# Kernel tuning notes

Measured on AMD Instinct MI355X. Metric: run time of the kernel, lower is better.

Reference implementation:

```python
import jax, jax.numpy as jnp
import numpy as np

B, IN_SEQ, TGT_SEQ = 128, 50, 25
IN_SIZE, OUT_SIZE, RNN = 128, 128, 2048


def setup_inputs() -> dict:
    key = jax.random.key(0)
    ks = jax.random.split(key, 10)
    s_in = 1.0 / np.sqrt(IN_SIZE)
    s_out = 1.0 / np.sqrt(OUT_SIZE)
    s_rnn = 1.0 / np.sqrt(RNN)
    return {
        "encoder_inputs": jax.random.normal(ks[0], (B, IN_SEQ, IN_SIZE), jnp.float32),
        "decoder_inputs": jax.random.normal(ks[1], (B, TGT_SEQ, IN_SIZE), jnp.float32),
        "fc1_w": jax.random.uniform(ks[2], (OUT_SIZE, IN_SIZE), jnp.float32, -s_in, s_in),
        "fc1_b": jax.random.uniform(ks[3], (OUT_SIZE,), jnp.float32, -s_in, s_in),
        "w_ih": jax.random.uniform(ks[4], (3 * RNN, OUT_SIZE), jnp.float32, -s_rnn, s_rnn),
        "w_hh": jax.random.uniform(ks[5], (3 * RNN, RNN), jnp.float32, -s_rnn, s_rnn),
        "b_ih": jax.random.uniform(ks[6], (3 * RNN,), jnp.float32, -s_rnn, s_rnn),
        "b_hh": jax.random.uniform(ks[7], (3 * RNN,), jnp.float32, -s_rnn, s_rnn),
        "fc2_w": jax.random.uniform(ks[8], (OUT_SIZE, RNN), jnp.float32, -s_rnn, s_rnn),
        "fc2_b": jax.random.uniform(ks[9], (OUT_SIZE,), jnp.float32, -s_rnn, s_rnn),
    }


def _gru_cell(x, h, w_ih, w_hh, b_ih, b_hh):
    # PyTorch GRUCell: gates ordered (r, z, n)
    gi = x @ w_ih.T + b_ih            # [B, 3R]
    gh = h @ w_hh.T + b_hh            # [B, 3R]
    i_r, i_z, i_n = jnp.split(gi, 3, axis=-1)
    h_r, h_z, h_n = jnp.split(gh, 3, axis=-1)
    r = jax.nn.sigmoid(i_r + h_r)
    z = jax.nn.sigmoid(i_z + h_z)
    n = jnp.tanh(i_n + r * h_n)
    return (1.0 - z) * n + z * h


def reference(encoder_inputs, decoder_inputs, fc1_w, fc1_b, w_ih, w_hh, b_ih, b_hh, fc2_w, fc2_b):
    # Eval mode: F.dropout(training=False) is identity.
    enc = encoder_inputs @ fc1_w.T + fc1_b              # [B, S_in, OUT]
    enc_t = jnp.transpose(enc, (1, 0, 2))               # time-major [S_in, B, OUT]
    h0 = jnp.zeros((encoder_inputs.shape[0], RNN), enc.dtype)

    def enc_step(state, x):
        return _gru_cell(x, state, w_ih, w_hh, b_ih, b_hh), None

    state, _ = jax.lax.scan(enc_step, h0, enc_t[:-1])   # input_seq - 1 steps

    def dec_step(carry, _):
        state, inp = carry
        inp = jax.lax.stop_gradient(inp)                # inp.detach()
        state = _gru_cell(inp, state, w_ih, w_hh, b_ih, b_hh)
        out = inp + state @ fc2_w.T + fc2_b             # residual decoder
        return (state, out), out

    _, outs = jax.lax.scan(dec_step, (state, enc_t[-1]), None, length=TGT_SEQ)
    return jnp.transpose(outs, (1, 0, 2))               # [B, TGT_SEQ, OUT]
```

## Files before the change

### kernel.cpp

```cpp
#include <hip/hip_runtime.h>
#include <limits.h>

constexpr int kB   = 128;
constexpr int kSin = 50;
constexpr int kT   = 25;
constexpr int kD   = 128;
constexpr int kR   = 2048;
constexpr int kNB  = 256;
constexpr int kNT  = 512;

typedef __bf16 bf16x8 __attribute__((ext_vector_type(8)));
typedef float  f32x4  __attribute__((ext_vector_type(4)));
typedef unsigned short u16;
typedef unsigned long long u64;

__device__ __forceinline__ float bf2f(u16 u){ union{unsigned i; float f;}x; x.i=((unsigned)u)<<16; return x.f; }
__device__ __forceinline__ u16 f2bf(float f){ union{float f; unsigned i;}x; x.f=f; return (u16)((x.i + 0x7FFFu + ((x.i>>16)&1u))>>16); }
__device__ __forceinline__ float sigm(float x){ return 1.f/(1.f+__expf(-x)); }

__device__ __forceinline__ void stg32(unsigned* p, unsigned v){
    __hip_atomic_store(p, v, __ATOMIC_RELAXED, __HIP_MEMORY_SCOPE_AGENT);
}
__device__ __forceinline__ void stg64(u64* p, u64 v){
    __hip_atomic_store(p, v, __ATOMIC_RELAXED, __HIP_MEMORY_SCOPE_AGENT);
}
__device__ __forceinline__ unsigned ald32(const void* p){
    return __hip_atomic_load((const unsigned*)p, __ATOMIC_RELAXED, __HIP_MEMORY_SCOPE_AGENT);
}
__device__ __forceinline__ u64 ald64(const void* p){
    return __hip_atomic_load((const u64*)p, __ATOMIC_RELAXED, __HIP_MEMORY_SCOPE_AGENT);
}
__device__ __forceinline__ bf16x8 ald128bf(const u16* p){
    union{ u64 q[2]; bf16x8 v; } t;
    t.q[0] = ald64(p);
    t.q[1] = ald64(p + 4);
    return t.v;
}
__device__ __forceinline__ float aldf(const float* p){
    union{ unsigned u; float f; } t; t.u = ald32(p); return t.f;
}

__device__ __forceinline__ bf16x8 pack8(float4 a, float4 b){
    union{ bf16x8 v; u16 u[8]; } t;
    t.u[0]=f2bf(a.x); t.u[1]=f2bf(a.y); t.u[2]=f2bf(a.z); t.u[3]=f2bf(a.w);
    t.u[4]=f2bf(b.x); t.u[5]=f2bf(b.y); t.u[6]=f2bf(b.z); t.u[7]=f2bf(b.w);
    return t.v;
}

__device__ __forceinline__ int pollflag(int* flags, int idx, int iter){
    if ((iter & 31) == 31) return atomicMax(&flags[idx*16], INT_MIN);
    return (int)ald32(&flags[idx*16]);
}
__device__ __forceinline__ void wait16(int* flags, int k, int base){
    const int lane = threadIdx.x & 63;
    for (int iter = 0;; ++iter){
        bool ok = true;
        if (lane < 16) ok = (pollflag(flags, base + lane, iter) >= k);
        if (__ballot(ok) == ~0ull) return;
        __builtin_amdgcn_s_sleep(1);
    }
}
__device__ __forceinline__ void wait128(int* flags, int k, int base){
    const int lane = threadIdx.x & 63;
    for (int iter = 0;; ++iter){
        bool ok = true;
#pragma unroll
        for (int j = 0; j < 2; ++j)
            ok &= (pollflag(flags, base + lane*2 + j, iter) >= k);
        if (__ballot(ok) == ~0ull) return;
        __builtin_amdgcn_s_sleep(1);
    }
}
__device__ __forceinline__ void arrive(int* flags, int k){
    __syncthreads();
    if (threadIdx.x == 0) atomicMax(&flags[blockIdx.x*16], k);
}

__device__ __forceinline__ void gbar(int* flags, int k, int base, int perlane)
{
    __syncthreads();
    const int tid = threadIdx.x;
    if (tid == 0) atomicMax(&flags[blockIdx.x*16], k);
    if (tid < 64) {
        int iter = 0;
        for (;;) {
            bool ok = true;
            for (int j = 0; j < perlane; ++j) {
                const int idx = base + tid*perlane + j;
                int v;
                if ((iter & 31) == 31) v = atomicMax(&flags[idx*16], INT_MIN);
                else                   v = (int)ald32(&flags[idx*16]);
                ok &= (v >= k);
            }
            if (__ballot(ok) == ~0ull) break;
            ++iter;
            __builtin_amdgcn_s_sleep(1);
        }
    }
    __syncthreads();
}

__device__ __forceinline__ void cvt_f32_bf16(const float* __restrict__ s, u16* __restrict__ d,
                                             int n4, int gtid, int gstride)
{
    for (int i = gtid; i < n4; i += gstride) {
        float4 v = ((const float4*)s)[i];
        u64 pk = (u64)f2bf(v.x) | ((u64)f2bf(v.y)<<16) | ((u64)f2bf(v.z)<<32) | ((u64)f2bf(v.w)<<48);
        stg64((u64*)d + i, pk);
    }
}

template<int NT, int NACC>
__device__ __forceinline__ void small_gemm(
    const u16* __restrict__ Am, int alda,
    const u16* __restrict__ Bp, int bldb,
    f32x4 (&acc)[NACC], u16* pool)
{
    const int tid=threadIdx.x, lane=tid&63, wv=tid>>6, g=wv>>2, mt=wv&3, ar=lane&15, aq=lane>>4;
    u16* sA = pool;
    u16* sB = pool + 8704;
    { int q=tid,     r=q>>4, c=q&15; *(uint4*)&sA[r*136+c*8] = *(const uint4*)(Am + r*alda + c*8); }
    { int q=tid+512, r=q>>4, c=q&15; *(uint4*)&sA[r*136+c*8] = *(const uint4*)(Am + r*alda + c*8); }
    for (int q=tid; q<NT*256; q+=kNT){
        int r=q>>4, c=q&15;
        *(uint4*)&sB[r*136+c*8] = *(const uint4*)(Bp + (size_t)r*bldb + c*8);
    }
    __syncthreads();
#pragma unroll
    for (int jt=0; jt<NT; ++jt){
        if ((jt&1) != g) continue;
#pragma unroll
        for (int kk=0; kk<4; ++kk){
            bf16x8 a = *(const bf16x8*)&sA[(mt*16+ar)*136 + kk*32 + aq*8];
            bf16x8 b = *(const bf16x8*)&sB[(jt*16+ar)*136 + kk*32 + aq*8];
            acc[jt>>1] = __builtin_amdgcn_mfma_f32_16x16x32_bf16(a,b,acc[jt>>1],0,0,0);
        }
    }
    __syncthreads();
}

__device__ __forceinline__ void gru_phase_flag(
    const u16* __restrict__ hcur, u16* __restrict__ hnxt,
    const u16* __restrict__ xb,
    const bf16x8 (&wB)[3][8], const bf16x8 (&wI)[3],
    const float4 b4, float (&hprev)[4],
    int wgc, int mrow0, u16* smem, u16* sH,
    int* flags, int hk, int xk, int fbase)
{
    const int tid=threadIdx.x, lane=tid&63, w=tid>>6, ar=lane&15, aq=lane>>4;
    const f32x4 zz = {0.f,0.f,0.f,0.f};
    f32x4 acc[3][4] = {{zz,zz,zz,zz},{zz,zz,zz,zz},{zz,zz,zz,zz}};
    f32x4 xn[4] = {zz,zz,zz,zz};

    if (hk) wait16(flags, hk, fbase + 16*w);

#pragma unroll
    for (int mt=0; mt<4; ++mt){
        const int row = mrow0 + mt*16 + ar;
        bf16x8 af[8];
#pragma unroll
        for (int c=0; c<8; ++c){
            const int s = 16*w + 2*c + (aq>>1);
            af[c] = ald128bf(hcur + (((s*128 + row)<<4) + (aq&1)*8));
        }
#pragma unroll
        for (int c=0; c<8; ++c){
            acc[0][mt] = __builtin_amdgcn_mfma_f32_16x16x32_bf16(af[c], wB[0][c], acc[0][mt],0,0,0);
            acc[1][mt] = __builtin_amdgcn_mfma_f32_16x16x32_bf16(af[c], wB[1][c], acc[1][mt],0,0,0);
            acc[2][mt] = __builtin_amdgcn_mfma_f32_16x16x32_bf16(af[c], wB[2][c], acc[2][mt],0,0,0);
        }
    }
    if (w < 4){
        if (xk) wait128(flags, xk, fbase);
#pragma unroll
        for (int mt=0; mt<4; ++mt){
            bf16x8 ax = ald128bf(xb + (mrow0+mt*16+ar)*kD + 32*w + aq*8);
            acc[0][mt] = __builtin_amdgcn_mfma_f32_16x16x32_bf16(ax, wI[0], acc[0][mt],0,0,0);
            acc[1][mt] = __builtin_amdgcn_mfma_f32_16x16x32_bf16(ax, wI[1], acc[1][mt],0,0,0);
            xn[mt]     = __builtin_amdgcn_mfma_f32_16x16x32_bf16(ax, wI[2], xn[mt],0,0,0);
        }
    }
    float* red = (float*)smem;
#define RCELL(wp,g4,mt) (red + (((((wp)*4+(g4))*4+(mt))*64 + lane)<<2))
    if (w >= 4){
#pragma unroll
        for (int g=0; g<3; ++g)
#pragma unroll
            for (int mt=0; mt<4; ++mt)
                *(f32x4*)RCELL(w-4, g, mt) = acc[g][mt];
    }
    __syncthreads();
    if (w < 4){
#pragma unroll
        for (int g=0; g<3; ++g)
#pragma unroll
            for (int mt=0; mt<4; ++mt)
                acc[g][mt] += *(f32x4*)RCELL(w, g, mt);
#pragma unroll
        for (int g=0; g<3; ++g)
#pragma unroll
            for (int mt=0; mt<4; ++mt)
                *(f32x4*)RCELL(w, g, mt) = acc[g][mt];
#pragma unroll
        for (int mt=0; mt<4; ++mt)
            *(f32x4*)RCELL(w, 3, mt) = xn[mt];
    }
    __syncthreads();
    if (tid < 256){
        const int mt = tid>>6, ls = tid&63, aqs = ls>>4, ars = ls&15;
        f32x4 R=zz, Z=zz, NH=zz, NX=zz;
#pragma unroll
        for (int wp=0; wp<4; ++wp){
            R  += *(f32x4*)(red + ((((wp*4+0)*4+mt)*64 + ls)<<2));
            Z  += *(f32x4*)(red + ((((wp*4+1)*4+mt)*64 + ls)<<2));
            NH += *(f32x4*)(red + ((((wp*4+2)*4+mt)*64 + ls)<<2));
            NX += *(f32x4*)(red + ((((wp*4+3)*4+mt)*64 + ls)<<2));
        }
#pragma unroll
        for (int rr=0; rr<4; ++rr){
            const int m = mrow0 + mt*16 + aqs*4 + rr;
            float r_ = sigm(R[rr] + b4.x);
            float z_ = sigm(Z[rr] + b4.y);
            float n_ = tanhf(NX[rr] + b4.z + r_*(NH[rr] + b4.w));
            float hn = (1.f-z_)*n_ + z_*hprev[rr];
            hprev[rr] = hn;
            u16 hb = f2bf(hn);
            sH[(mt*16 + aqs*4 + rr)*16 + ars] = hb;
            unsigned other = (unsigned)__shfl_xor((int)(unsigned)hb, 1);
            if (!(ars&1))
                stg32((unsigned*)(hnxt + ((wgc*128+m)<<4) + ars), (unsigned)hb | (other<<16));
        }
    }
#undef RCELL
    __syncthreads();
}

__device__ __forceinline__ void fc2_partial(
    const u16* __restrict__ sH, const bf16x8 (&wF2)[4],
    int wgc, int mh, float* __restrict__ part)
{
    const int tid=threadIdx.x, lane=tid&63, w=tid>>6, ar=lane&15, aq=lane>>4;
    const int mt = w&3, nh = w>>2;
    bf16x8 a;
    if (aq < 2) a = *(const bf16x8*)&sH[(mt*16+ar)*16 + aq*8];
    else {
#pragma unroll
        for (int i=0;i<8;++i) a[i] = (__bf16)0.f;
    }
    const f32x4 zz = {0.f,0.f,0.f,0.f};
    f32x4 acc[4] = {zz,zz,zz,zz};
#pragma unroll
    for (int j=0;j<4;++j)
        acc[j] = __builtin_amdgcn_mfma_f32_16x16x32_bf16(a, wF2[j], acc[j],0,0,0);
#pragma unroll
    for (int j=0;j<4;++j){
        const int col = (nh*4+j)*16 + ar;
#pragma unroll
        for (int rr=0;rr<4;++rr){
            const int row = mt*16 + aq*4 + rr;
            stg32((unsigned*)(part + ((((size_t)mh*64+row)*128 + wgc)*128 + col)),
                  __float_as_uint(acc[j][rr]));
        }
    }
}

__global__ __launch_bounds__(kNT, 2) void seq2seq_kernel(
    const void* __restrict__ enc_in_raw, const void* __restrict__ fc1_w_raw,
    const void* __restrict__ fc1_b_raw,  const void* __restrict__ w_ih_raw,
    const void* __restrict__ w_hh_raw,   const void* __restrict__ b_ih_raw,
    const void* __restrict__ b_hh_raw,   const void* __restrict__ fc2_w_raw,
    const void* __restrict__ fc2_b_raw,
    void* __restrict__ out_raw,
    u16* __restrict__ enc_act,
    u16* __restrict__ h_b16,
    u16* __restrict__ inp_b16,
    float* __restrict__ inp_f32,
    float* __restrict__ encF,
    float* __restrict__ bias,
    float* __restrict__ part,
    int* flags,
    u16* __restrict__ cv_encx, u16* __restrict__ cv_fc2, u16* __restrict__ cv_fc1)
{
    __shared__ __align__(16) u16 smem[33792];
    __shared__ int sflag;
    u16* sH = smem + 32768;
    const int wg = blockIdx.x, tid = threadIdx.x;
    const int wgc = wg & 127, mrow0 = (wg >> 7) * 64;
    const int lane = tid & 63, wv = tid >> 6, ar = lane & 15, aq = lane >> 4;
    const int gtid = wg * kNT + tid, gstride = kNB * kNT;
    const int dom = (wg >> 7) * 128;

    {
        const u16* p = (const u16*)enc_in_raw;
        int found = 0;
        for (int i = tid; i < 16384; i += kNT) found |= ((p[i] & 0x7F80) == 0x7F80) ? 1 : 0;
        if (tid == 0) sflag = 0;
        __syncthreads();
        if (found) sflag = 1;
        __syncthreads();
    }
    const bool F32 = (sflag != 0);

    bf16x8 wB[3][8];
    bf16x8 wI[3];
    {
        const int w4 = wv & 3;
        if (F32){
            const float* Wh = (const float*)w_hh_raw;
            const float* Wi = (const float*)w_ih_raw;
#pragma unroll
            for (int g=0; g<3; ++g)
#pragma unroll
                for (int c=0; c<8; ++c){
                    size_t o = (size_t)(g*kR + wgc*16 + ar)*kR + 256*wv + 32*c + aq*8;
                    wB[g][c] = pack8(*(const float4*)(Wh+o), *(const float4*)(Wh+o+4));
                }
#pragma unroll
            for (int g=0; g<3; ++g){
                size_t o = (size_t)(g*kR + wgc*16 + ar)*kD + 32*w4 + aq*8;
                wI[g] = pack8(*(const float4*)(Wi+o), *(const float4*)(Wi+o+4));
            }
        } else {
            const u16* Wh = (const u16*)w_hh_raw;
            const u16* Wi = (const u16*)w_ih_raw;
#pragma unroll
            for (int g=0; g<3; ++g)
#pragma unroll
                for (int c=0; c<8; ++c)
                    wB[g][c] = *(const bf16x8*)(Wh + (size_t)(g*kR + wgc*16 + ar)*kR + 256*wv + 32*c + aq*8);
#pragma unroll
            for (int g=0; g<3; ++g)
                wI[g] = *(const bf16x8*)(Wi + (size_t)(g*kR + wgc*16 + ar)*kD + 32*w4 + aq*8);
        }
    }

    if (F32) {
        cvt_f32_bf16((const float*)fc2_w_raw, cv_fc2,  (kD*kR)/4,       gtid, gstride);
        cvt_f32_bf16((const float*)fc1_w_raw, cv_fc1,  (kD*kD)/4,       gtid, gstride);
        cvt_f32_bf16((const float*)enc_in_raw,cv_encx, (kB*kSin*kD)/4,  gtid, gstride);
        for (int i = gtid; i < 3*kR; i += gstride) {
            stg32((unsigned*)&bias[i],        __float_as_uint(((const float*)b_ih_raw)[i]));
            stg32((unsigned*)&bias[3*kR + i], __float_as_uint(((const float*)b_hh_raw)[i]));
        }
        for (int i = gtid; i < kD; i += gstride) {
            stg32((unsigned*)&bias[6*kR + i],      __float_as_uint(((const float*)fc1_b_raw)[i]));
            stg32((unsigned*)&bias[6*kR + kD + i], __float_as_uint(((const float*)fc2_b_raw)[i]));
        }
    } else {
        for (int i = gtid; i < 3*kR; i += gstride) {
            stg32((unsigned*)&bias[i],        __float_as_uint(bf2f(((const u16*)b_ih_raw)[i])));
            stg32((unsigned*)&bias[3*kR + i], __float_as_uint(bf2f(((const u16*)b_hh_raw)[i])));
        }
        for (int i = gtid; i < kD; i += gstride) {
            stg32((unsigned*)&bias[6*kR + i],      __float_as_uint(bf2f(((const u16*)fc1_b_raw)[i])));
            stg32((unsigned*)&bias[6*kR + kD + i], __float_as_uint(bf2f(((const u16*)fc2_b_raw)[i])));
        }
    }
    for (int i = gtid; i < (kB*kR)/2; i += gstride) stg32((unsigned*)h_b16 + i, 0u);
    gbar(flags, 1, 0, 4);

    const u16* ENCX = F32 ? cv_encx : (const u16*)enc_in_raw;
    const u16* WF2  = F32 ? cv_fc2  : (const u16*)fc2_w_raw;
    const u16* WF1  = F32 ? cv_fc1  : (const u16*)fc1_w_raw;

    float4 b4;
    {
        const int hc = wgc*16 + ar;
        b4.x = aldf(&bias[hc])      + aldf(&bias[3*kR+hc]);
        b4.y = aldf(&bias[kR+hc])   + aldf(&bias[4*kR+hc]);
        b4.z = aldf(&bias[2*kR+hc]);
        b4.w = aldf(&bias[5*kR+hc]);
    }
    bf16x8 wF2[4];
    {
        const int nh = wv>>2;
#pragma unroll
        for (int j=0;j<4;++j){
            if (aq < 2)
                wF2[j] = ald128bf(WF2 + (size_t)((nh*4+j)*16+ar)*kR + wgc*16 + aq*8);
            else {
#pragma unroll
                for (int i=0;i<8;++i) wF2[j][i] = (__bf16)0.f;
            }
        }
    }
    const float fc2b = aldf(&bias[6*kR + kD + (wg&1)*64 + (tid&63)]);
    float hprev[4] = {0.f, 0.f, 0.f, 0.f};

    if (wgc < kSin) {
        const int g = wv>>2, mt = wv&3;
        const f32x4 zz = {0.f,0.f,0.f,0.f};
        f32x4 ae[4] = {zz,zz,zz,zz};
        small_gemm<8,4>(ENCX + ((size_t)mrow0*kSin + wgc)*kD, kSin*kD, WF1, kD, ae, smem);
#pragma unroll
        for (int jt=0; jt<8; ++jt){
            if ((jt&1) != g) continue;
            int col = jt*16 + ar;
            float fb = aldf(&bias[6*kR + col]);
#pragma unroll
            for (int rr=0; rr<4; ++rr){
                int m = mrow0 + mt*16 + aq*4 + rr;
                float v = ae[jt>>1][rr] + fb;
                u16 hb = f2bf(v);
                unsigned other = (unsigned)__shfl_xor((int)(unsigned)hb, 1);
                if (!(ar&1))
                    stg32((unsigned*)(enc_act + ((size_t)wgc*kB + m)*kD + col),
                          (unsigned)hb | (other<<16));
                if (wgc == kSin-1)
                    stg32((unsigned*)(encF + (size_t)m*kD + col), __float_as_uint(v));
            }
        }
    }
    gbar(flags, 2, dom, 2);

    int par = 0;
    for (int t = 0; t < kSin-1; ++t) {
        gru_phase_flag(h_b16 + (size_t)par*kB*kR, h_b16 + (size_t)(1-par)*kB*kR,
                       enc_act + (size_t)t*kB*kD, wB, wI, b4, hprev, wgc, mrow0, smem, sH,
                       flags, (t==0 ? 0 : t+2), 0, dom);
        arrive(flags, t+3);
        par ^= 1;
    }

    const u16*   ib  = enc_act + (size_t)(kSin-1)*kB*kD;
    const float* ifp = encF;
    const int mh = wg >> 7;
    for (int d = 0; d < kT; ++d) {
        gru_phase_flag(h_b16 + (size_t)par*kB*kR, h_b16 + (size_t)(1-par)*kB*kR,
                       ib, wB, wI, b4, hprev, wgc, mrow0, smem, sH,
                       flags, (d==0 ? 51 : 50+2*d), (d==0 ? 0 : 51+2*d), dom);
        fc2_partial(sH, wF2, wgc, mh, part);
        arrive(flags, 52+2*d);
        par ^= 1;

        u16*   nib = inp_b16 + (size_t)(d&1)*kB*kD;
        float* nif = inp_f32 + (size_t)(d&1)*kB*kD;
        wait128(flags, 52+2*d, dom);
        {
            const int row = wg >> 1, ch = wg & 1;
            const int mh2 = row >> 6, rl = row & 63;
            const float* pr = part + (size_t)((mh2*64 + rl)*128)*128;
            const int cl = tid & 63, sg = tid >> 6;
            float s = 0.f;
#pragma unroll
            for (int j=0;j<16;++j) s += aldf(&pr[(size_t)(sg*16+j)*128 + ch*64 + cl]);
            float* red2 = (float*)smem;
            red2[sg*64 + cl] = s;
            __syncthreads();
            if (tid < 64){
                float t2 = 0.f;
#pragma unroll
                for (int g2=0; g2<8; ++g2) t2 += red2[g2*64 + tid];
                const int colg = ch*64 + tid;
                const float o = t2 + fc2b + aldf(&ifp[(size_t)row*kD + colg]);
                const size_t ob = ((size_t)row*kT + d)*kD + colg;
                if (F32) ((float*)out_raw)[ob] = o;
                else     ((u16*)out_raw)[ob]   = f2bf(o);
                stg32((unsigned*)(nif + (size_t)row*kD + colg), __float_as_uint(o));
                u16 hb = f2bf(o);
                unsigned other = (unsigned)__shfl_xor((int)(unsigned)hb, 1);
                if (!(tid&1))
                    stg32((unsigned*)(nib + (size_t)row*kD + colg), (unsigned)hb | (other<<16));
            }
        }
        arrive(flags, 53+2*d);
        ib = nib; ifp = nif;
    }
}

extern "C" void kernel_launch(void* const* d_in, const int* in_sizes, int n_in,
                              void* d_out, int out_size, void* d_ws, size_t ws_size,
                              hipStream_t stream)
{
    size_t off = 0;
    char* ws = (char*)d_ws;
    auto alloc = [&](size_t bytes) -> char* {
        char* p = ws + off;
        off = (off + bytes + 255) & ~(size_t)255;
        return p;
    };
    u16*   enc_act = (u16*)alloc((size_t)kSin*kB*kD*2);
    u16*   h_b16   = (u16*)alloc((size_t)2*kB*kR*2);
    u16*   inp_b16 = (u16*)alloc((size_t)2*kB*kD*2);
    float* inp_f32 = (float*)alloc((size_t)2*kB*kD*4);
    float* encF    = (float*)alloc((size_t)kB*kD*4);
    float* bias    = (float*)alloc((size_t)(6*kR + 2*kD)*4);
    float* part    = (float*)alloc((size_t)2*64*128*128*4);
    int*   flags   = (int*)alloc((size_t)kNB*16*4);
    u16*   cv_encx = (u16*)alloc((size_t)kB*kSin*kD*2);
    u16*   cv_fc2  = (u16*)alloc((size_t)kD*kR*2);
    u16*   cv_fc1  = (u16*)alloc((size_t)kD*kD*2);
    (void)ws_size; (void)in_sizes; (void)n_in; (void)out_size;

    seq2seq_kernel<<<dim3(kNB), dim3(kNT), 0, stream>>>(
        d_in[0], d_in[2], d_in[3], d_in[4], d_in[5], d_in[6], d_in[7], d_in[8], d_in[9],
        d_out,
        enc_act, h_b16, inp_b16, inp_f32, encF, bias, part, flags,
        cv_encx, cv_fc2, cv_fc1);
}
```

Baseline: 1.537 ms.

## Use 8-slot hidden-state ring with plain loads and periodic acquire fences

Switches the hidden-state and decoder-input double buffers to an 8-deep ring. This lets the per-step hidden and input reads use ordinary cached vector loads instead of relaxed agent-scope atomic loads, with an acquire fence only when the ring wraps. The aim is to cut the latency of the atomic 128-bit loads on the critical recurrent path. The risk is correctness: this relies on stale cache lines never being hit for fresh slots. Only the ring zero slot is initialized, and the flag waits themselves may not order the plain loads.

```diff
diff --git a/kernel.cpp b/kernel.cpp
--- a/kernel.cpp
+++ b/kernel.cpp
@@ -8,6 +8,7 @@
 constexpr int kR   = 2048;
 constexpr int kNB  = 256;
 constexpr int kNT  = 512;
+constexpr int kRing = 8;
 
 typedef __bf16 bf16x8 __attribute__((ext_vector_type(8)));
 typedef float  f32x4  __attribute__((ext_vector_type(4)));
@@ -145,13 +146,15 @@
     const bf16x8 (&wB)[3][8], const bf16x8 (&wI)[3],
     const float4 b4, float (&hprev)[4],
     int wgc, int mrow0, u16* smem, u16* sH,
-    int* flags, int hk, int xk, int fbase)
+    int* flags, int hk, int xk, int fbase, bool dofence)
 {
     const int tid=threadIdx.x, lane=tid&63, w=tid>>6, ar=lane&15, aq=lane>>4;
     const f32x4 zz = {0.f,0.f,0.f,0.f};
     f32x4 acc[3][4] = {{zz,zz,zz,zz},{zz,zz,zz,zz},{zz,zz,zz,zz}};
     f32x4 xn[4] = {zz,zz,zz,zz};
 
+    if (dofence) __builtin_amdgcn_fence(__ATOMIC_ACQUIRE, "agent");
+
     if (hk) wait16(flags, hk, fbase + 16*w);
 
 #pragma unroll
@@ -161,7 +164,7 @@
 #pragma unroll
         for (int c=0; c<8; ++c){
             const int s = 16*w + 2*c + (aq>>1);
-            af[c] = ald128bf(hcur + (((s*128 + row)<<4) + (aq&1)*8));
+            af[c] = *(const bf16x8*)(hcur + (((s*128 + row)<<4) + (aq&1)*8));
         }
 #pragma unroll
         for (int c=0; c<8; ++c){
@@ -174,7 +177,7 @@
         if (xk) wait128(flags, xk, fbase);
 #pragma unroll
         for (int mt=0; mt<4; ++mt){
-            bf16x8 ax = ald128bf(xb + (mrow0+mt*16+ar)*kD + 32*w + aq*8);
+            bf16x8 ax = *(const bf16x8*)(xb + (mrow0+mt*16+ar)*kD + 32*w + aq*8);
             acc[0][mt] = __builtin_amdgcn_mfma_f32_16x16x32_bf16(ax, wI[0], acc[0][mt],0,0,0);
             acc[1][mt] = __builtin_amdgcn_mfma_f32_16x16x32_bf16(ax, wI[1], acc[1][mt],0,0,0);
             xn[mt]     = __builtin_amdgcn_mfma_f32_16x16x32_bf16(ax, wI[2], xn[mt],0,0,0);
@@ -289,6 +292,7 @@
     const int lane = tid & 63, wv = tid >> 6, ar = lane & 15, aq = lane >> 4;
     const int gtid = wg * kNT + tid, gstride = kNB * kNT;
     const int dom = (wg >> 7) * 128;
+    const size_t HS = (size_t)kB*kR;
 
     {
         const u16* p = (const u16*)enc_in_raw;
@@ -356,7 +360,7 @@
             stg32((unsigned*)&bias[6*kR + kD + i], __float_as_uint(bf2f(((const u16*)fc2_b_raw)[i])));
         }
     }
-    for (int i = gtid; i < (kB*kR)/2; i += gstride) stg32((unsigned*)h_b16 + i, 0u);
+    for (int i = gtid; i < (int)((kB*kR)/2); i += gstride) stg32((unsigned*)h_b16 + i, 0u);
     gbar(flags, 1, 0, 4);
 
     const u16* ENCX = F32 ? cv_encx : (const u16*)enc_in_raw;
@@ -413,28 +417,28 @@
     }
     gbar(flags, 2, dom, 2);
 
-    int par = 0;
     for (int t = 0; t < kSin-1; ++t) {
-        gru_phase_flag(h_b16 + (size_t)par*kB*kR, h_b16 + (size_t)(1-par)*kB*kR,
+        gru_phase_flag(h_b16 + (size_t)(t & 7)*HS, h_b16 + (size_t)((t+1) & 7)*HS,
                        enc_act + (size_t)t*kB*kD, wB, wI, b4, hprev, wgc, mrow0, smem, sH,
-                       flags, (t==0 ? 0 : t+2), 0, dom);
+                       flags, (t==0 ? 0 : t+2), 0, dom,
+                       (t > 0) && ((t & 7) == 0));
         arrive(flags, t+3);
-        par ^= 1;
     }
 
     const u16*   ib  = enc_act + (size_t)(kSin-1)*kB*kD;
     const float* ifp = encF;
     const int mh = wg >> 7;
     for (int d = 0; d < kT; ++d) {
-        gru_phase_flag(h_b16 + (size_t)par*kB*kR, h_b16 + (size_t)(1-par)*kB*kR,
+        const int g = 49 + d;
+        gru_phase_flag(h_b16 + (size_t)(g & 7)*HS, h_b16 + (size_t)((g+1) & 7)*HS,
                        ib, wB, wI, b4, hprev, wgc, mrow0, smem, sH,
-                       flags, (d==0 ? 51 : 50+2*d), (d==0 ? 0 : 51+2*d), dom);
+                       flags, (d==0 ? 51 : 50+2*d), (d==0 ? 0 : 51+2*d), dom,
+                       (g & 7) == 0);
         fc2_partial(sH, wF2, wgc, mh, part);
         arrive(flags, 52+2*d);
-        par ^= 1;
-
-        u16*   nib = inp_b16 + (size_t)(d&1)*kB*kD;
-        float* nif = inp_f32 + (size_t)(d&1)*kB*kD;
+
+        u16*   nib = inp_b16 + (size_t)(d & 7)*kB*kD;
+        float* nif = inp_f32 + (size_t)(d & 7)*kB*kD;
         wait128(flags, 52+2*d, dom);
         {
             const int row = wg >> 1, ch = wg & 1;
@@ -452,7 +456,7 @@
 #pragma unroll
                 for (int g2=0; g2<8; ++g2) t2 += red2[g2*64 + tid];
                 const int colg = ch*64 + tid;
-                const float o = t2 + fc2b + aldf(&ifp[(size_t)row*kD + colg]);
+                const float o = t2 + fc2b + ifp[(size_t)row*kD + colg];
                 const size_t ob = ((size_t)row*kT + d)*kD + colg;
                 if (F32) ((float*)out_raw)[ob] = o;
                 else     ((u16*)out_raw)[ob]   = f2bf(o);
@@ -480,9 +484,9 @@
         return p;
     };
     u16*   enc_act = (u16*)alloc((size_t)kSin*kB*kD*2);
-    u16*   h_b16   = (u16*)alloc((size_t)2*kB*kR*2);
-    u16*   inp_b16 = (u16*)alloc((size_t)2*kB*kD*2);
-    float* inp_f32 = (float*)alloc((size_t)2*kB*kD*4);
+    u16*   h_b16   = (u16*)alloc((size_t)kRing*kB*kR*2);
+    u16*   inp_b16 = (u16*)alloc((size_t)kRing*kB*kD*2);
+    float* inp_f32 = (float*)alloc((size_t)kRing*kB*kD*4);
     float* encF    = (float*)alloc((size_t)kB*kD*4);
     float* bias    = (float*)alloc((size_t)(6*kR + 2*kD)*4);
     float* part    = (float*)alloc((size_t)2*64*128*128*4);
```

Result: no change. 1.531 ms (-0.4%).
